# Performance work log

Hardware: AMD Instinct MI355X
Metric: run time of the kernel (lower is better)

## Reference

```python
import jax, jax.numpy as jnp
import numpy as np

N_NODES = 100000
N_EDGES = 1600000
IN_FEATS = 128
N_HIDDEN = 128
N_CLASSES = 47


def setup_inputs() -> dict:
    key = jax.random.key(0)
    ks = jax.random.split(key, 12)
    def lin(k, fi, fo):
        s = 1.0 / np.sqrt(fi)
        return jax.random.uniform(k, (fi, fo), jnp.float32, -s, s)
    return {
        "x": jax.random.normal(ks[0], (N_NODES, IN_FEATS), jnp.float32),
        "src": jax.random.randint(ks[1], (N_EDGES,), 0, N_NODES, jnp.int32),
        "dst": jax.random.randint(ks[2], (N_EDGES,), 0, N_NODES, jnp.int32),
        "W_self0": lin(ks[3], IN_FEATS, N_HIDDEN),
        "W_neigh0": lin(ks[4], IN_FEATS, N_HIDDEN),
        "b0": jnp.zeros((N_HIDDEN,), jnp.float32),
        "W_self1": lin(ks[5], N_HIDDEN, N_HIDDEN),
        "W_neigh1": lin(ks[6], N_HIDDEN, N_HIDDEN),
        "b1": jnp.zeros((N_HIDDEN,), jnp.float32),
        "W_self2": lin(ks[7], N_HIDDEN, N_CLASSES),
        "W_neigh2": lin(ks[8], N_HIDDEN, N_CLASSES),
        "b2": jnp.zeros((N_CLASSES,), jnp.float32),
    }


def _sage_layer(h, src, dst, W_self, W_neigh, b):
    # DGL SAGEConv 'mean': fc_self(h_dst) + fc_neigh(mean of in-neighbor feats) + bias
    agg = jax.ops.segment_sum(h[src], dst, num_segments=N_NODES)  # [N, d]
    deg = jax.ops.segment_sum(jnp.ones((src.shape[0],), h.dtype), dst,
                              num_segments=N_NODES)
    h_neigh = agg / jnp.maximum(deg, 1.0)[:, None]
    return h @ W_self + h_neigh @ W_neigh + b


def reference(x, src, dst, W_self0, W_neigh0, b0, W_self1, W_neigh1, b1,
              W_self2, W_neigh2, b2):
    h = _sage_layer(x, src, dst, W_self0, W_neigh0, b0)
    h = jax.nn.relu(h)
    h = _sage_layer(h, src, dst, W_self1, W_neigh1, b1)
    h = jax.nn.relu(h)
    h = _sage_layer(h, src, dst, W_self2, W_neigh2, b2)
    return h
```

## Files before the change

kernel.cpp:

```cpp
#include <hip/hip_runtime.h>

#define NN 100000
#define NE 1600000
#define NBK 391
#define CHUNK 8192
#define NBLK ((NE + CHUNK - 1) / CHUNK)
#define MPAD 100096
#define CASTB 12500
#define PREPB (CASTB + 128 + 128 + 48)
#define GBLK 2048
#define NPW ((NN + 8191) / 8192)

using bf16x8 = __attribute__((ext_vector_type(8))) short;
using f32x4  = __attribute__((ext_vector_type(4))) float;

typedef const __attribute__((address_space(1))) unsigned int* gas_t;
typedef __attribute__((address_space(3))) unsigned int* las_t;

static __device__ __forceinline__ unsigned short f2bf(float f) {
    unsigned int u = __float_as_uint(f);
    unsigned int r = (u + 0x7FFFu + ((u >> 16) & 1u)) >> 16;
    return (unsigned short)r;
}
static __device__ __forceinline__ float lo16(unsigned int u) {
    return __uint_as_float(u << 16);
}
static __device__ __forceinline__ float hi16(unsigned int u) {
    return __uint_as_float(u & 0xFFFF0000u);
}
static __device__ __forceinline__ unsigned int pk(float lo, float hi) {
    return ((unsigned int)f2bf(hi) << 16) | (unsigned int)f2bf(lo);
}


__global__ __launch_bounds__(256) void k_hist_prep(
        const int* __restrict__ dst, int* __restrict__ ghist,
        const float4* __restrict__ x4, ushort4* __restrict__ XB4,
        const float* __restrict__ Ws0, const float* __restrict__ Wn0,
        unsigned short* __restrict__ BT0,
        const float* __restrict__ Ws1, const float* __restrict__ Wn1,
        unsigned short* __restrict__ BT1,
        const float* __restrict__ Ws2, const float* __restrict__ Wn2,
        unsigned short* __restrict__ BT2) {
    __shared__ int h[NBK];
    int bid = blockIdx.x, t = threadIdx.x;
    if (bid < NBLK) {
        for (int i = t; i < NBK; i += 256) h[i] = 0;
        __syncthreads();
        int beg = bid * CHUNK, end = min(beg + CHUNK, NE);
        for (int i = beg + t; i < end; i += 256)
            atomicAdd(&h[dst[i] >> 8], 1);
        __syncthreads();
        for (int i = t; i < NBK; i += 256) ghist[bid * NBK + i] = h[i];
        return;
    }
    int pb = bid - NBLK;
    if (pb < CASTB) {
        int i = pb * 256 + t;
        float4 v = x4[i];
        ushort4 o;
        o.x = f2bf(v.x); o.y = f2bf(v.y); o.z = f2bf(v.z); o.w = f2bf(v.w);
        XB4[i] = o;
    } else if (pb < CASTB + 128) {
        int idx = (pb - CASTB) * 256 + t;
        int k = idx >> 7, n = idx & 127;
        float v = (k < 128) ? Ws0[k * 128 + n] : Wn0[(k - 128) * 128 + n];
        BT0[n * 256 + k] = f2bf(v);
    } else if (pb < CASTB + 256) {
        int idx = (pb - CASTB - 128) * 256 + t;
        int k = idx >> 7, n = idx & 127;
        float v = (k < 128) ? Ws1[k * 128 + n] : Wn1[(k - 128) * 128 + n];
        BT1[n * 256 + k] = f2bf(v);
    } else {
        int idx = (pb - CASTB - 256) * 256 + t;
        if (idx < 96 * 128) {
            int n = idx >> 7, k = idx & 127;
            float v = 0.f;
            if (n < 48) { if (n < 47) v = Ws2[k * 47 + n]; }
            else        { int cc = n - 48; if (cc < 47) v = Wn2[k * 47 + cc]; }
            BT2[n * 128 + k] = f2bf(v);
        }
    }
}

__global__ __launch_bounds__(512) void k_basescan(const int* __restrict__ ghist,
                                                  int* __restrict__ boff,
                                                  int* __restrict__ gbase) {
    __shared__ int s[512];
    int t = threadIdx.x;
    int tot = 0;
    if (t < NBK) {
#pragma unroll 4
        for (int blk = 0; blk < NBLK; ++blk) tot += ghist[blk * NBK + t];
    }
    s[t] = tot;
    __syncthreads();
    for (int o = 1; o < 512; o <<= 1) {
        int u = (t >= o) ? s[t - o] : 0;
        __syncthreads();
        s[t] += u;
        __syncthreads();
    }
    int base = s[t] - tot;
    if (t <= NBK) boff[t] = base;
    if (t < NBK) {
        int run = base;
        for (int blk = 0; blk < NBLK; ++blk) {
            int g = ghist[blk * NBK + t];
            gbase[blk * NBK + t] = run;
            run += g;
        }
    }
}

__global__ __launch_bounds__(256) void k_scatter(const int* __restrict__ src,
                                                 const int* __restrict__ dst,
                                                 const int* __restrict__ gbase,
                                                 unsigned int* __restrict__ eb) {
    __shared__ int cur[NBK];
    int b = blockIdx.x, t = threadIdx.x;
    for (int i = t; i < NBK; i += 256) cur[i] = gbase[b * NBK + i];
    __syncthreads();
    int beg = b * CHUNK, end = min(beg + CHUNK, NE);
    for (int i = beg + t; i < end; i += 256) {
        int d = dst[i];
        int p = atomicAdd(&cur[d >> 8], 1);
        eb[p] = ((unsigned int)(d & 255) << 24) | (unsigned int)src[i];
    }
}

__global__ __launch_bounds__(256) void k_csr(const unsigned int* __restrict__ eb,
                                             const int* __restrict__ boff,
                                             int* __restrict__ rp,
                                             int* __restrict__ col) {
    __shared__ int h[256];
    __shared__ int sc[256];
    __shared__ int cur[256];
    int b = blockIdx.x, t = threadIdx.x;
    h[t] = 0;
    __syncthreads();
    int beg = boff[b], end = boff[b + 1];
    for (int e = beg + t; e < end; e += 256)
        atomicAdd(&h[eb[e] >> 24], 1);
    __syncthreads();
    int c = h[t];
    sc[t] = c;
    __syncthreads();
    for (int o = 1; o < 256; o <<= 1) {
        int v = (t >= o) ? sc[t - o] : 0;
        __syncthreads();
        sc[t] += v;
        __syncthreads();
    }
    int excl = beg + sc[t] - c;
    int node = (b << 8) + t;
    if (node < NN) rp[node] = excl;
    if (node == NN - 1) rp[NN] = NE;
    cur[t] = excl;
    __syncthreads();
    for (int e = beg + t; e < end; e += 256) {
        unsigned int p = eb[e];
        int pos = atomicAdd(&cur[p >> 24], 1);
        col[pos] = (int)(p & 0xFFFFFFu);
    }
}


__global__ __launch_bounds__(256) void k_gather128(
        const uint4* __restrict__ hb4,
        const int* __restrict__ rp, const int* __restrict__ col,
        uint4* __restrict__ hnb4) {
    int wave = blockIdx.x * 4 + (threadIdx.x >> 6);
    int lane = threadIdx.x & 63;
    int q = lane >> 4, l16 = lane & 15;
    int n0 = wave * NPW;
    int n1 = min(n0 + NPW, NN);
    for (int node = n0; node < n1; ++node) {
        int beg = rp[node], end = rp[node + 1];
        float a0 = 0.f, a1 = 0.f, a2 = 0.f, a3 = 0.f;
        float a4 = 0.f, a5 = 0.f, a6 = 0.f, a7 = 0.f;
        float b0 = 0.f, b1 = 0.f, b2 = 0.f, b3 = 0.f;
        float b4 = 0.f, b5 = 0.f, b6 = 0.f, b7 = 0.f;
        int e = beg;
        for (; e + 8 <= end; e += 8) {
            int c0 = col[e + q];
            int c1 = col[e + 4 + q];
            uint4 v0 = hb4[(size_t)c0 * 16 + l16];
            uint4 v1 = hb4[(size_t)c1 * 16 + l16];
            a0 += lo16(v0.x); a1 += hi16(v0.x); a2 += lo16(v0.y); a3 += hi16(v0.y);
            a4 += lo16(v0.z); a5 += hi16(v0.z); a6 += lo16(v0.w); a7 += hi16(v0.w);
            b0 += lo16(v1.x); b1 += hi16(v1.x); b2 += lo16(v1.y); b3 += hi16(v1.y);
            b4 += lo16(v1.z); b5 += hi16(v1.z); b6 += lo16(v1.w); b7 += hi16(v1.w);
        }
        for (; e < end; e += 4) {
            if (e + q < end) {
                uint4 v = hb4[(size_t)col[e + q] * 16 + l16];
                a0 += lo16(v.x); a1 += hi16(v.x); a2 += lo16(v.y); a3 += hi16(v.y);
                a4 += lo16(v.z); a5 += hi16(v.z); a6 += lo16(v.w); a7 += hi16(v.w);
            }
        }
        float s0 = a0 + b0, s1 = a1 + b1, s2 = a2 + b2, s3 = a3 + b3;
        float s4 = a4 + b4, s5 = a5 + b5, s6 = a6 + b6, s7 = a7 + b7;
        s0 += __shfl_xor(s0, 16); s0 += __shfl_xor(s0, 32);
        s1 += __shfl_xor(s1, 16); s1 += __shfl_xor(s1, 32);
        s2 += __shfl_xor(s2, 16); s2 += __shfl_xor(s2, 32);
        s3 += __shfl_xor(s3, 16); s3 += __shfl_xor(s3, 32);
        s4 += __shfl_xor(s4, 16); s4 += __shfl_xor(s4, 32);
        s5 += __shfl_xor(s5, 16); s5 += __shfl_xor(s5, 32);
        s6 += __shfl_xor(s6, 16); s6 += __shfl_xor(s6, 32);
        s7 += __shfl_xor(s7, 16); s7 += __shfl_xor(s7, 32);
        if (q == 0) {
            float d = (float)(end - beg);
            float inv = (d > 0.f) ? 1.0f / d : 0.0f;
            uint4 o;
            o.x = pk(s0 * inv, s1 * inv);
            o.y = pk(s2 * inv, s3 * inv);
            o.z = pk(s4 * inv, s5 * inv);
            o.w = pk(s6 * inv, s7 * inv);
            hnb4[(size_t)node * 16 + l16] = o;
        }
    }
}


__global__ __launch_bounds__(256, 2) void k_mgemm(
        const unsigned short* __restrict__ A0,
        const unsigned short* __restrict__ A1,
        const unsigned short* __restrict__ BT,
        const float* __restrict__ bias,
        unsigned short* __restrict__ outB) {
    __shared__ char sA[34816];
    unsigned short* hl = (unsigned short*)sA;
    int t = threadIdx.x;
    int lane = t & 63, wid = t >> 6;
    int wm = wid >> 1, wn = wid & 1;
    int lr = lane & 15, lg = lane >> 4;
    int brow = blockIdx.x * 128;
    int colw = wn * 64;
    f32x4 zero = {0.f, 0.f, 0.f, 0.f};
    f32x4 acc[4][4];
#pragma unroll
    for (int a = 0; a < 4; ++a)
#pragma unroll
        for (int b = 0; b < 4; ++b) acc[a][b] = zero;

#pragma unroll 1
    for (int p = 0; p < 2; ++p) {
        const unsigned short* A = p ? A1 : A0;
#pragma unroll
        for (int it = 0; it < 8; ++it) {
            int rl = wid * 32 + it * 4 + (lane >> 4);
            int ch = (lane & 15) ^ (rl & 7);
            const char* src = (const char*)A + (size_t)(brow + rl) * 256 + ch * 16;
            __builtin_amdgcn_global_load_lds((gas_t)src,
                (las_t)(sA + wid * 8192 + it * 1024), 16, 0, 0);
        }
        __syncthreads();
        bf16x8 bReg[4][4];
#pragma unroll
        for (int nf = 0; nf < 4; ++nf)
#pragma unroll
            for (int ks = 0; ks < 4; ++ks)
                bReg[nf][ks] = *(const bf16x8*)&BT[(size_t)(colw + nf * 16 + lr) * 256 + p * 128 + ks * 32 + lg * 8];
#pragma unroll
        for (int mf = 0; mf < 4; ++mf) {
            int rl = wm * 64 + mf * 16 + lr;
            bf16x8 aReg[4];
#pragma unroll
            for (int ks = 0; ks < 4; ++ks)
                aReg[ks] = *(const bf16x8*)&sA[rl * 256 + (((ks * 4 + lg) ^ (rl & 7)) << 4)];
#pragma unroll
            for (int ks = 0; ks < 4; ++ks)
#pragma unroll
                for (int nf = 0; nf < 4; ++nf)
                    acc[mf][nf] = __builtin_amdgcn_mfma_f32_16x16x32_bf16(
                        aReg[ks], bReg[nf][ks], acc[mf][nf], 0, 0, 0);
        }
        __syncthreads();
    }
#pragma unroll
    for (int nf = 0; nf < 4; ++nf) {
        int cidx = colw + nf * 16 + lr;
        float bb = bias[cidx];
#pragma unroll
        for (int mf = 0; mf < 4; ++mf) {
#pragma unroll
            for (int j = 0; j < 4; ++j) {
                int lrow = wm * 64 + mf * 16 + lg * 4 + j;
                hl[lrow * 136 + cidx] = f2bf(fmaxf(acc[mf][nf][j] + bb, 0.f));
            }
        }
    }
    __syncthreads();
    uint4* ob4 = (uint4*)outB;
#pragma unroll
    for (int i = 0; i < 8; ++i) {
        int idx = i * 256 + t;
        int row = idx >> 4, c = idx & 15;
        uint4 val = *(const uint4*)&hl[row * 136 + c * 8];
        ob4[(size_t)(brow + row) * 16 + c] = val;
    }
}


__global__ __launch_bounds__(256, 2) void k_mgemm_l12(
        const unsigned short* __restrict__ A0,
        const unsigned short* __restrict__ A1,
        const unsigned short* __restrict__ BT,
        const float* __restrict__ bias,
        const unsigned short* __restrict__ BT2,
        const float* __restrict__ bias2,
        float* __restrict__ S,
        unsigned short* __restrict__ TB) {
    __shared__ char buf[34816];
    unsigned short* hl = (unsigned short*)buf;
    unsigned short* tb = (unsigned short*)buf;
    int t = threadIdx.x;
    int lane = t & 63, wid = t >> 6;
    int wm = wid >> 1, wn = wid & 1;
    int lr = lane & 15, lg = lane >> 4;
    int brow = blockIdx.x * 128;
    int colw = wn * 64;
    f32x4 zero = {0.f, 0.f, 0.f, 0.f};
    f32x4 acc[4][4];
#pragma unroll
    for (int a = 0; a < 4; ++a)
#pragma unroll
        for (int b = 0; b < 4; ++b) acc[a][b] = zero;

#pragma unroll 1
    for (int p = 0; p < 2; ++p) {
        const unsigned short* A = p ? A1 : A0;
#pragma unroll
        for (int it = 0; it < 8; ++it) {
            int rl = wid * 32 + it * 4 + (lane >> 4);
            int ch = (lane & 15) ^ (rl & 7);
            const char* src = (const char*)A + (size_t)(brow + rl) * 256 + ch * 16;
            __builtin_amdgcn_global_load_lds((gas_t)src,
                (las_t)(buf + wid * 8192 + it * 1024), 16, 0, 0);
        }
        __syncthreads();
        bf16x8 bReg[4][4];
#pragma unroll
        for (int nf = 0; nf < 4; ++nf)
#pragma unroll
            for (int ks = 0; ks < 4; ++ks)
                bReg[nf][ks] = *(const bf16x8*)&BT[(size_t)(colw + nf * 16 + lr) * 256 + p * 128 + ks * 32 + lg * 8];
#pragma unroll
        for (int mf = 0; mf < 4; ++mf) {
            int rl = wm * 64 + mf * 16 + lr;
            bf16x8 aReg[4];
#pragma unroll
            for (int ks = 0; ks < 4; ++ks)
                aReg[ks] = *(const bf16x8*)&buf[rl * 256 + (((ks * 4 + lg) ^ (rl & 7)) << 4)];
#pragma unroll
            for (int ks = 0; ks < 4; ++ks)
#pragma unroll
                for (int nf = 0; nf < 4; ++nf)
                    acc[mf][nf] = __builtin_amdgcn_mfma_f32_16x16x32_bf16(
                        aReg[ks], bReg[nf][ks], acc[mf][nf], 0, 0, 0);
        }
        __syncthreads();
    }
#pragma unroll
    for (int nf = 0; nf < 4; ++nf) {
        int cidx = colw + nf * 16 + lr;
        float bb = bias[cidx];
#pragma unroll
        for (int mf = 0; mf < 4; ++mf) {
#pragma unroll
            for (int j = 0; j < 4; ++j) {
                int lrow = wm * 64 + mf * 16 + lg * 4 + j;
                hl[lrow * 136 + cidx] = f2bf(fmaxf(acc[mf][nf][j] + bb, 0.f));
            }
        }
    }
    __syncthreads();
    int colw2 = wn * 48;
    f32x4 acc2[4][3];
#pragma unroll
    for (int a = 0; a < 4; ++a)
#pragma unroll
        for (int b = 0; b < 3; ++b) acc2[a][b] = zero;
    bf16x8 bReg2[3][4];
#pragma unroll
    for (int nf = 0; nf < 3; ++nf)
#pragma unroll
        for (int ks = 0; ks < 4; ++ks)
            bReg2[nf][ks] = *(const bf16x8*)&BT2[(size_t)(colw2 + nf * 16 + lr) * 128 + ks * 32 + lg * 8];
#pragma unroll
    for (int mf = 0; mf < 4; ++mf) {
        int rl = wm * 64 + mf * 16 + lr;
        bf16x8 aReg[4];
#pragma unroll
        for (int ks = 0; ks < 4; ++ks)
            aReg[ks] = *(const bf16x8*)&hl[rl * 136 + ks * 32 + lg * 8];
#pragma unroll
        for (int ks = 0; ks < 4; ++ks)
#pragma unroll
            for (int nf = 0; nf < 3; ++nf)
                acc2[mf][nf] = __builtin_amdgcn_mfma_f32_16x16x32_bf16(
                    aReg[ks], bReg2[nf][ks], acc2[mf][nf], 0, 0, 0);
    }
#pragma unroll
    for (int nf = 0; nf < 3; ++nf) {
        int cidx = colw2 + nf * 16 + lr;
#pragma unroll
        for (int mf = 0; mf < 4; ++mf) {
#pragma unroll
            for (int j = 0; j < 4; ++j) {
                int row = brow + wm * 64 + mf * 16 + lg * 4 + j;
                if (row < NN && cidx < 47)
                    S[(size_t)row * 48 + cidx] = acc2[mf][nf][j] + bias2[cidx];
            }
        }
    }
    __syncthreads();
    if (wn == 1) {
#pragma unroll
        for (int nf = 0; nf < 3; ++nf) {
            int cc = nf * 16 + lr;
#pragma unroll
            for (int mf = 0; mf < 4; ++mf) {
#pragma unroll
                for (int j = 0; j < 4; ++j) {
                    int lrow = wm * 64 + mf * 16 + lg * 4 + j;
                    tb[lrow * 72 + cc] = f2bf(acc2[mf][nf][j]);
                }
            }
        }
    }
    for (int i = t; i < 128 * 16; i += 256) {
        int row = i >> 4, c = 48 + (i & 15);
        tb[row * 72 + c] = 0;
    }
    __syncthreads();
    uint4* tb4 = (uint4*)TB;
#pragma unroll
    for (int i = 0; i < 4; ++i) {
        int idx = i * 256 + t;
        int row = idx >> 3, c = idx & 7;
        uint4 val = *(const uint4*)&tb[row * 72 + c * 8];
        tb4[(size_t)(brow + row) * 8 + c] = val;
    }
}


__global__ __launch_bounds__(256) void k_gather47(
        const uint2* __restrict__ TB2,
        const float4* __restrict__ S4,
        const int* __restrict__ rp, const int* __restrict__ col,
        float* __restrict__ out) {
    int wave = blockIdx.x * 4 + (threadIdx.x >> 6);
    int lane = threadIdx.x & 63;
    int q = lane >> 4, l16 = lane & 15;
    int n0 = wave * NPW;
    int n1 = min(n0 + NPW, NN);
    for (int node = n0; node < n1; ++node) {
        int beg = rp[node], end = rp[node + 1];
        float a0 = 0.f, a1 = 0.f, a2 = 0.f, a3 = 0.f;
        float b0 = 0.f, b1 = 0.f, b2 = 0.f, b3 = 0.f;
        int e = beg;
        for (; e + 8 <= end; e += 8) {
            int i0 = col[e + q];
            int i1 = col[e + 4 + q];
            uint2 u0 = TB2[(size_t)i0 * 16 + l16];
            uint2 u1 = TB2[(size_t)i1 * 16 + l16];
            a0 += lo16(u0.x); a1 += hi16(u0.x); a2 += lo16(u0.y); a3 += hi16(u0.y);
            b0 += lo16(u1.x); b1 += hi16(u1.x); b2 += lo16(u1.y); b3 += hi16(u1.y);
        }
        for (; e < end; e += 4) {
            if (e + q < end) {
                uint2 u = TB2[(size_t)col[e + q] * 16 + l16];
                a0 += lo16(u.x); a1 += hi16(u.x); a2 += lo16(u.y); a3 += hi16(u.y);
            }
        }
        float s0 = a0 + b0, s1 = a1 + b1, s2 = a2 + b2, s3 = a3 + b3;
        s0 += __shfl_xor(s0, 16); s0 += __shfl_xor(s0, 32);
        s1 += __shfl_xor(s1, 16); s1 += __shfl_xor(s1, 32);
        s2 += __shfl_xor(s2, 16); s2 += __shfl_xor(s2, 32);
        s3 += __shfl_xor(s3, 16); s3 += __shfl_xor(s3, 32);
        if (q == 0 && l16 < 12) {
            float d = (float)(end - beg);
            float inv = (d > 0.f) ? 1.0f / d : 0.0f;
            float4 sv = S4[(size_t)node * 12 + l16];
            int c = l16 * 4;
            out[(size_t)node * 47 + c]     = sv.x + s0 * inv;
            out[(size_t)node * 47 + c + 1] = sv.y + s1 * inv;
            out[(size_t)node * 47 + c + 2] = sv.z + s2 * inv;
            if (c + 3 < 47) out[(size_t)node * 47 + c + 3] = sv.w + s3 * inv;
        }
    }
}


static inline size_t align_up(size_t x, size_t a) { return (x + a - 1) / a * a; }

extern "C" void kernel_launch(void* const* d_in, const int* in_sizes, int n_in,
                              void* d_out, int out_size, void* d_ws, size_t ws_size,
                              hipStream_t stream) {
    const float* x   = (const float*)d_in[0];
    const int* src   = (const int*)d_in[1];
    const int* dst   = (const int*)d_in[2];
    const float* Ws0 = (const float*)d_in[3];
    const float* Wn0 = (const float*)d_in[4];
    const float* b0  = (const float*)d_in[5];
    const float* Ws1 = (const float*)d_in[6];
    const float* Wn1 = (const float*)d_in[7];
    const float* b1  = (const float*)d_in[8];
    const float* Ws2 = (const float*)d_in[9];
    const float* Wn2 = (const float*)d_in[10];
    const float* b2  = (const float*)d_in[11];
    float* out = (float*)d_out;

    char* ws = (char*)d_ws;
    size_t off = 0;
    auto alloc = [&](size_t bytes) -> void* {
        void* p = ws + off; off = align_up(off + bytes, 256); return p;
    };
    int* row_ptr = (int*)alloc((size_t)(NN + 1) * 4);
    int* boff    = (int*)alloc((size_t)(NBK + 1) * 4);
    int* gbase   = (int*)alloc((size_t)NBLK * NBK * 4);
    int* ghist   = (int*)alloc((size_t)NBLK * NBK * 4);
    int* col     = (int*)alloc((size_t)NE * 4);
    unsigned short* XB  = (unsigned short*)alloc((size_t)MPAD * 128 * 2);
    unsigned short* BT0 = (unsigned short*)alloc(128 * 256 * 2);
    unsigned short* BT1 = (unsigned short*)alloc(128 * 256 * 2);
    unsigned short* BT2 = (unsigned short*)alloc(96 * 128 * 2);
    unsigned int* HNB   = (unsigned int*)alloc((size_t)MPAD * 128 * 2);
    size_t sbytes  = (size_t)NN * 48 * 4;
    size_t tbbytes = (size_t)MPAD * 64 * 2;
    char* stb = (char*)alloc(sbytes + tbbytes);
    unsigned int* eb   = (unsigned int*)stb;
    float* S           = (float*)stb;
    unsigned short* TB = (unsigned short*)(stb + sbytes);

    k_hist_prep<<<NBLK + PREPB, 256, 0, stream>>>(
        dst, ghist, (const float4*)x, (ushort4*)XB,
        Ws0, Wn0, BT0, Ws1, Wn1, BT1, Ws2, Wn2, BT2);
    k_basescan<<<1, 512, 0, stream>>>(ghist, boff, gbase);
    k_scatter<<<NBLK, 256, 0, stream>>>(src, dst, gbase, eb);
    k_csr<<<NBK, 256, 0, stream>>>(eb, boff, row_ptr, col);

    int mgrid = MPAD / 128;

    k_gather128<<<GBLK, 256, 0, stream>>>((const uint4*)XB, row_ptr, col, (uint4*)HNB);
    k_mgemm<<<mgrid, 256, 0, stream>>>(XB, (const unsigned short*)HNB, BT0, b0, XB);
    k_gather128<<<GBLK, 256, 0, stream>>>((const uint4*)XB, row_ptr, col, (uint4*)HNB);
    k_mgemm_l12<<<mgrid, 256, 0, stream>>>(XB, (const unsigned short*)HNB, BT1, b1,
                                           BT2, b2, S, TB);
    k_gather47<<<GBLK, 256, 0, stream>>>((const uint2*)TB, (const float4*)S,
                                         row_ptr, col, out);
}
```

Before: 317.5 us.

## Split gather kernels into feature slices across blocks for per-XCD L2 locality

The two gather kernels now split each row's features into column slices: 4 slices of 32 bf16 for the 128-wide gather, 2 slices for the 47-class gather. Each block owns one slice of a small node chunk, so every lane loads one dword per edge instead of a uint4 or uint2. Consecutive block IDs (b&7) map to slice/chunk pairs, so the blocks sharing a slice appear meant to land on the same XCD, shrinking each L2's working set to a fraction of the feature table. The inner loop is also unrolled to 16 edges to keep more loads in flight. The cost is narrower per-lane loads and reading the col indices several times, once per slice.

Result: slower. 495.3 us (+56.0%).

```diff
diff --git a/kernel.cpp b/kernel.cpp
--- a/kernel.cpp
+++ b/kernel.cpp
@@ -8,8 +8,9 @@
 #define MPAD 100096
 #define CASTB 12500
 #define PREPB (CASTB + 128 + 128 + 48)
-#define GBLK 2048
-#define NPW ((NN + 8191) / 8192)
+#define GBLK 8192
+#define NCH 49
+#define NCH47 25
 
 using bf16x8 = __attribute__((ext_vector_type(8))) short;
 using f32x4  = __attribute__((ext_vector_type(4))) float;
@@ -167,57 +168,61 @@
 
 
 __global__ __launch_bounds__(256) void k_gather128(
-        const uint4* __restrict__ hb4,
+        const unsigned int* __restrict__ hbu,
         const int* __restrict__ rp, const int* __restrict__ col,
-        uint4* __restrict__ hnb4) {
-    int wave = blockIdx.x * 4 + (threadIdx.x >> 6);
+        unsigned int* __restrict__ hnbu) {
+    int b = blockIdx.x;
+    int slot = b & 7;
+    int soff = (slot & 3) * 16;
+    int chunk = ((b >> 3) << 1) | (slot >> 2);
+    int wv = threadIdx.x >> 6;
     int lane = threadIdx.x & 63;
     int q = lane >> 4, l16 = lane & 15;
-    int n0 = wave * NPW;
-    int n1 = min(n0 + NPW, NN);
+    int cbeg = chunk * NCH;
+    int cend = min(cbeg + NCH, NN);
+    int n0 = cbeg + wv * 13;
+    int n1 = min(n0 + 13, cend);
     for (int node = n0; node < n1; ++node) {
         int beg = rp[node], end = rp[node + 1];
-        float a0 = 0.f, a1 = 0.f, a2 = 0.f, a3 = 0.f;
-        float a4 = 0.f, a5 = 0.f, a6 = 0.f, a7 = 0.f;
-        float b0 = 0.f, b1 = 0.f, b2 = 0.f, b3 = 0.f;
-        float b4 = 0.f, b5 = 0.f, b6 = 0.f, b7 = 0.f;
+        float a0 = 0.f, a1 = 0.f, b0 = 0.f, b1 = 0.f;
+        float c0 = 0.f, c1 = 0.f, d0 = 0.f, d1 = 0.f;
         int e = beg;
+        for (; e + 16 <= end; e += 16) {
+            int i0 = col[e + q];
+            int i1 = col[e + 4 + q];
+            int i2 = col[e + 8 + q];
+            int i3 = col[e + 12 + q];
+            unsigned int v0 = hbu[(size_t)i0 * 64 + soff + l16];
+            unsigned int v1 = hbu[(size_t)i1 * 64 + soff + l16];
+            unsigned int v2 = hbu[(size_t)i2 * 64 + soff + l16];
+            unsigned int v3 = hbu[(size_t)i3 * 64 + soff + l16];
+            a0 += lo16(v0); a1 += hi16(v0);
+            b0 += lo16(v1); b1 += hi16(v1);
+            c0 += lo16(v2); c1 += hi16(v2);
+            d0 += lo16(v3); d1 += hi16(v3);
+        }
         for (; e + 8 <= end; e += 8) {
-            int c0 = col[e + q];
-            int c1 = col[e + 4 + q];
-            uint4 v0 = hb4[(size_t)c0 * 16 + l16];
-            uint4 v1 = hb4[(size_t)c1 * 16 + l16];
-            a0 += lo16(v0.x); a1 += hi16(v0.x); a2 += lo16(v0.y); a3 += hi16(v0.y);
-            a4 += lo16(v0.z); a5 += hi16(v0.z); a6 += lo16(v0.w); a7 += hi16(v0.w);
-            b0 += lo16(v1.x); b1 += hi16(v1.x); b2 += lo16(v1.y); b3 += hi16(v1.y);
-            b4 += lo16(v1.z); b5 += hi16(v1.z); b6 += lo16(v1.w); b7 += hi16(v1.w);
+            int i0 = col[e + q];
+            int i1 = col[e + 4 + q];
+            unsigned int v0 = hbu[(size_t)i0 * 64 + soff + l16];
+            unsigned int v1 = hbu[(size_t)i1 * 64 + soff + l16];
+            a0 += lo16(v0); a1 += hi16(v0);
+            b0 += lo16(v1); b1 += hi16(v1);
         }
         for (; e < end; e += 4) {
             if (e + q < end) {
-                uint4 v = hb4[(size_t)col[e + q] * 16 + l16];
-                a0 += lo16(v.x); a1 += hi16(v.x); a2 += lo16(v.y); a3 += hi16(v.y);
-                a4 += lo16(v.z); a5 += hi16(v.z); a6 += lo16(v.w); a7 += hi16(v.w);
+                unsigned int v = hbu[(size_t)col[e + q] * 64 + soff + l16];
+                a0 += lo16(v); a1 += hi16(v);
             }
         }
-        float s0 = a0 + b0, s1 = a1 + b1, s2 = a2 + b2, s3 = a3 + b3;
-        float s4 = a4 + b4, s5 = a5 + b5, s6 = a6 + b6, s7 = a7 + b7;
+        float s0 = (a0 + b0) + (c0 + d0);
+        float s1 = (a1 + b1) + (c1 + d1);
         s0 += __shfl_xor(s0, 16); s0 += __shfl_xor(s0, 32);
         s1 += __shfl_xor(s1, 16); s1 += __shfl_xor(s1, 32);
-        s2 += __shfl_xor(s2, 16); s2 += __shfl_xor(s2, 32);
-        s3 += __shfl_xor(s3, 16); s3 += __shfl_xor(s3, 32);
-        s4 += __shfl_xor(s4, 16); s4 += __shfl_xor(s4, 32);
-        s5 += __shfl_xor(s5, 16); s5 += __shfl_xor(s5, 32);
-        s6 += __shfl_xor(s6, 16); s6 += __shfl_xor(s6, 32);
-        s7 += __shfl_xor(s7, 16); s7 += __shfl_xor(s7, 32);
         if (q == 0) {
             float d = (float)(end - beg);
             float inv = (d > 0.f) ? 1.0f / d : 0.0f;
-            uint4 o;
-            o.x = pk(s0 * inv, s1 * inv);
-            o.y = pk(s2 * inv, s3 * inv);
-            o.z = pk(s4 * inv, s5 * inv);
-            o.w = pk(s6 * inv, s7 * inv);
-            hnb4[(size_t)node * 16 + l16] = o;
+            hnbu[(size_t)node * 64 + soff + l16] = pk(s0 * inv, s1 * inv);
         }
     }
 }
@@ -447,48 +452,66 @@
 
 
 __global__ __launch_bounds__(256) void k_gather47(
-        const uint2* __restrict__ TB2,
-        const float4* __restrict__ S4,
+        const unsigned int* __restrict__ TBu,
+        const float2* __restrict__ S2,
         const int* __restrict__ rp, const int* __restrict__ col,
         float* __restrict__ out) {
-    int wave = blockIdx.x * 4 + (threadIdx.x >> 6);
+    int b = blockIdx.x;
+    int slot = b & 7;
+    int slice = slot & 1;
+    int soff = slice * 16;
+    int chunk = ((b >> 3) << 2) | (slot >> 1);
+    int wv = threadIdx.x >> 6;
     int lane = threadIdx.x & 63;
     int q = lane >> 4, l16 = lane & 15;
-    int n0 = wave * NPW;
-    int n1 = min(n0 + NPW, NN);
+    int cbeg = chunk * NCH47;
+    int cend = min(cbeg + NCH47, NN);
+    int n0 = cbeg + wv * 7;
+    int n1 = min(n0 + 7, cend);
     for (int node = n0; node < n1; ++node) {
         int beg = rp[node], end = rp[node + 1];
-        float a0 = 0.f, a1 = 0.f, a2 = 0.f, a3 = 0.f;
-        float b0 = 0.f, b1 = 0.f, b2 = 0.f, b3 = 0.f;
+        float a0 = 0.f, a1 = 0.f, b0 = 0.f, b1 = 0.f;
+        float c0 = 0.f, c1 = 0.f, d0 = 0.f, d1 = 0.f;
         int e = beg;
+        for (; e + 16 <= end; e += 16) {
+            int i0 = col[e + q];
+            int i1 = col[e + 4 + q];
+            int i2 = col[e + 8 + q];
+            int i3 = col[e + 12 + q];
+            unsigned int v0 = TBu[(size_t)i0 * 32 + soff + l16];
+            unsigned int v1 = TBu[(size_t)i1 * 32 + soff + l16];
+            unsigned int v2 = TBu[(size_t)i2 * 32 + soff + l16];
+            unsigned int v3 = TBu[(size_t)i3 * 32 + soff + l16];
+            a0 += lo16(v0); a1 += hi16(v0);
+            b0 += lo16(v1); b1 += hi16(v1);
+            c0 += lo16(v2); c1 += hi16(v2);
+            d0 += lo16(v3); d1 += hi16(v3);
+        }
         for (; e + 8 <= end; e += 8) {
             int i0 = col[e + q];
             int i1 = col[e + 4 + q];
-            uint2 u0 = TB2[(size_t)i0 * 16 + l16];
-            uint2 u1 = TB2[(size_t)i1 * 16 + l16];
-            a0 += lo16(u0.x); a1 += hi16(u0.x); a2 += lo16(u0.y); a3 += hi16(u0.y);
-            b0 += lo16(u1.x); b1 += hi16(u1.x); b2 += lo16(u1.y); b3 += hi16(u1.y);
+            unsigned int v0 = TBu[(size_t)i0 * 32 + soff + l16];
+            unsigned int v1 = TBu[(size_t)i1 * 32 + soff + l16];
+            a0 += lo16(v0); a1 += hi16(v0);
+            b0 += lo16(v1); b1 += hi16(v1);
         }
         for (; e < end; e += 4) {
             if (e + q < end) {
-                uint2 u = TB2[(size_t)col[e + q] * 16 + l16];
-                a0 += lo16(u.x); a1 += hi16(u.x); a2 += lo16(u.y); a3 += hi16(u.y);
+                unsigned int v = TBu[(size_t)col[e + q] * 32 + soff + l16];
+                a0 += lo16(v); a1 += hi16(v);
             }
         }
-        float s0 = a0 + b0, s1 = a1 + b1, s2 = a2 + b2, s3 = a3 + b3;
+        float s0 = (a0 + b0) + (c0 + d0);
+        float s1 = (a1 + b1) + (c1 + d1);
         s0 += __shfl_xor(s0, 16); s0 += __shfl_xor(s0, 32);
         s1 += __shfl_xor(s1, 16); s1 += __shfl_xor(s1, 32);
-        s2 += __shfl_xor(s2, 16); s2 += __shfl_xor(s2, 32);
-        s3 += __shfl_xor(s3, 16); s3 += __shfl_xor(s3, 32);
-        if (q == 0 && l16 < 12) {
+        int c = slice * 32 + l16 * 2;
+        if (q == 0 && c < 47) {
             float d = (float)(end - beg);
             float inv = (d > 0.f) ? 1.0f / d : 0.0f;
-            float4 sv = S4[(size_t)node * 12 + l16];
-            int c = l16 * 4;
-            out[(size_t)node * 47 + c]     = sv.x + s0 * inv;
-            out[(size_t)node * 47 + c + 1] = sv.y + s1 * inv;
-            out[(size_t)node * 47 + c + 2] = sv.z + s2 * inv;
-            if (c + 3 < 47) out[(size_t)node * 47 + c + 3] = sv.w + s3 * inv;
+            float2 sv = S2[(size_t)node * 24 + soff + l16];
+            out[(size_t)node * 47 + c] = sv.x + s0 * inv;
+            if (c + 1 < 47) out[(size_t)node * 47 + c + 1] = sv.y + s1 * inv;
         }
     }
 }
@@ -544,11 +567,13 @@
 
     int mgrid = MPAD / 128;
 
-    k_gather128<<<GBLK, 256, 0, stream>>>((const uint4*)XB, row_ptr, col, (uint4*)HNB);
+    k_gather128<<<GBLK, 256, 0, stream>>>((const unsigned int*)XB, row_ptr, col,
+                                          (unsigned int*)HNB);
     k_mgemm<<<mgrid, 256, 0, stream>>>(XB, (const unsigned short*)HNB, BT0, b0, XB);
-    k_gather128<<<GBLK, 256, 0, stream>>>((const uint4*)XB, row_ptr, col, (uint4*)HNB);
+    k_gather128<<<GBLK, 256, 0, stream>>>((const unsigned int*)XB, row_ptr, col,
+                                          (unsigned int*)HNB);
     k_mgemm_l12<<<mgrid, 256, 0, stream>>>(XB, (const unsigned short*)HNB, BT1, b1,
                                            BT2, b2, S, TB);
-    k_gather47<<<GBLK, 256, 0, stream>>>((const uint2*)TB, (const float4*)S,
+    k_gather47<<<GBLK, 256, 0, stream>>>((const unsigned int*)TB, (const float2*)S,
                                          row_ptr, col, out);
 }
```
